# Kernel tuning notes

Hardware: AMD Instinct MI355X
Metric: run time of the kernel (lower is better)

The kernel has to match this reference:

```python
import jax, jax.numpy as jnp
import numpy as np

N = 2_000_000
IN_CH = 10
UNITS = 32  # out_channels // 2 since last_vfe=False
KMAX = 64   # voxel coordinate range per axis


def setup_inputs() -> dict:
    key = jax.random.key(0)
    k1, k2, k3, k4, k5, k6, k7 = jax.random.split(key, 7)
    return {
        "inputs": jax.random.normal(k1, (N, IN_CH), dtype=jnp.float32),
        "mean": jax.random.normal(k2, (N, 6), dtype=jnp.float32),
        "linear_w": jax.random.normal(k3, (IN_CH, UNITS), dtype=jnp.float32) * 0.1,
        "linear_b": jax.random.normal(k4, (UNITS,), dtype=jnp.float32) * 0.1,
        "weight_w": jax.random.normal(k5, (6, UNITS), dtype=jnp.float32) * 0.1,
        "weight_b": jax.random.normal(k6, (UNITS,), dtype=jnp.float32) * 0.1,
        "bxyz_indx": jax.random.randint(k7, (N, 4), 0, KMAX, dtype=jnp.int32),
    }


def _encode_rows(bxyz_indx):
    # unique-by-row is equivalent to unique on a collision-free scalar key;
    # scatter_max-then-gather is invariant to how unique ids are labeled.
    b = bxyz_indx.astype(jnp.int64)
    return ((b[:, 0] * KMAX + b[:, 1]) * KMAX + b[:, 2]) * KMAX + b[:, 3]


def reference(inputs, mean, linear_w, linear_b, weight_w, weight_b, bxyz_indx):
    # x = relu(Linear(inputs)); gating by relu(Linear(mean))  (activate=True, gs=None)
    x = jax.nn.relu(inputs @ linear_w + linear_b)          # [N, UNITS]
    x_weight = jax.nn.relu(mean @ weight_w + weight_b)     # [N, UNITS]
    x = x * x_weight
    # unique voxel id per point -> inverse indices (jit-safe fixed size)
    keys = _encode_rows(bxyz_indx)
    _, inv = jnp.unique(keys, return_inverse=True, size=keys.shape[0], fill_value=-1)
    inv = inv.reshape(-1)
    # scatter_max over voxels, then gather back per point
    max_feature = jax.ops.segment_max(x, inv, num_segments=keys.shape[0])
    gather_max = max_feature[inv, :]                       # [N, UNITS]
    return jnp.concatenate([x, gather_max], axis=1)        # [N, 2*UNITS]
```

## Files before the change

### kernel.cpp

```cpp
#include <hip/hip_runtime.h>
#include <stdint.h>

#define IN_CH   10
#define MEAN_CH 6
#define UNITS   32
#define EMPTY_KEY  ((int)0xAAAAAAAA)
#define MULTI_FLAG 0x40000000

typedef float f32x4 __attribute__((ext_vector_type(4)));

__global__ __launch_bounds__(256) void vfe_hash_insert(
    const int* __restrict__ bxyz, int* __restrict__ keytab,
    unsigned char* __restrict__ multi, int* __restrict__ slots,
    unsigned hmask, int hshift, int nrows)
{
    int row = blockIdx.x * blockDim.x + threadIdx.x;
    if (row >= nrows) return;
    const int4 b = *(const int4*)(bxyz + (size_t)row * 4);
    int key = ((b.x * 64 + b.y) * 64 + b.z) * 64 + b.w;
    unsigned h = ((unsigned)key * 2654435761u) >> hshift;
    h &= hmask;
    while (true) {
        int old = atomicCAS(&keytab[h], EMPTY_KEY, key);
        if (old == EMPTY_KEY) break;
        if (old == key) { multi[h] = 1; break; }
        h = (h + 1) & hmask;
    }
    slots[row] = (int)h;
}

__global__ __launch_bounds__(256) void vfe_compute(
    const float* __restrict__ inputs, const float* __restrict__ mean,
    const float* __restrict__ W1, const float* __restrict__ b1,
    const float* __restrict__ W2, const float* __restrict__ b2,
    int* __restrict__ slots, const unsigned char* __restrict__ multi,
    float* __restrict__ out, int* __restrict__ maxtab, int nrows)
{
    int tid = blockIdx.x * blockDim.x + threadIdx.x;
    int row = tid >> 3;
    int c4  = (tid & 7) * 4;
    if (row >= nrows) return;

    const float* __restrict__ in_row = inputs + (size_t)row * IN_CH;
    const float* __restrict__ mn_row = mean   + (size_t)row * MEAN_CH;

    float4 bb1 = *(const float4*)(b1 + c4);
    float a0 = bb1.x, a1 = bb1.y, a2 = bb1.z, a3 = bb1.w;
#pragma unroll
    for (int k = 0; k < IN_CH; ++k) {
        float v = in_row[k];
        float4 w = *(const float4*)(W1 + k * UNITS + c4);
        a0 = fmaf(v, w.x, a0); a1 = fmaf(v, w.y, a1);
        a2 = fmaf(v, w.z, a2); a3 = fmaf(v, w.w, a3);
    }
    a0 = fmaxf(a0, 0.0f); a1 = fmaxf(a1, 0.0f);
    a2 = fmaxf(a2, 0.0f); a3 = fmaxf(a3, 0.0f);

    float4 bb2 = *(const float4*)(b2 + c4);
    float g0 = bb2.x, g1 = bb2.y, g2 = bb2.z, g3 = bb2.w;
#pragma unroll
    for (int k = 0; k < MEAN_CH; ++k) {
        float v = mn_row[k];
        float4 w = *(const float4*)(W2 + k * UNITS + c4);
        g0 = fmaf(v, w.x, g0); g1 = fmaf(v, w.y, g1);
        g2 = fmaf(v, w.z, g2); g3 = fmaf(v, w.w, g3);
    }
    g0 = fmaxf(g0, 0.0f); g1 = fmaxf(g1, 0.0f);
    g2 = fmaxf(g2, 0.0f); g3 = fmaxf(g3, 0.0f);

    f32x4 x;
    x.x = a0 * g0; x.y = a1 * g1; x.z = a2 * g2; x.w = a3 * g3;

    f32x4* o0 = (f32x4*)(out + (size_t)row * 64 + c4);
    f32x4* o1 = (f32x4*)(out + (size_t)row * 64 + 32 + c4);
    __builtin_nontemporal_store(x, o0);
    __builtin_nontemporal_store(x, o1);

    int slotv = slots[row];
    if (multi[slotv]) {
        int* __restrict__ mt = maxtab + (size_t)slotv * UNITS + c4;
        atomicMax(mt + 0, (int)__float_as_uint(x.x));
        atomicMax(mt + 1, (int)__float_as_uint(x.y));
        atomicMax(mt + 2, (int)__float_as_uint(x.z));
        atomicMax(mt + 3, (int)__float_as_uint(x.w));
        if ((tid & 7) == 0)
            slots[row] = slotv | MULTI_FLAG;
    }
}

__global__ __launch_bounds__(256) void vfe_fixup(
    const int* __restrict__ slots, const int* __restrict__ maxtab,
    float* __restrict__ out, int nrows)
{
    int row = blockIdx.x * blockDim.x + threadIdx.x;
    if (row >= nrows) return;
    int v = slots[row];
    if (!(v & MULTI_FLAG)) return;
    int slot = v & ~MULTI_FLAG;
    const f32x4* src = (const f32x4*)(maxtab + (size_t)slot * UNITS);
    f32x4* dst = (f32x4*)(out + (size_t)row * 64 + 32);
#pragma unroll
    for (int i = 0; i < 8; ++i) dst[i] = src[i];
}

extern "C" void kernel_launch(void* const* d_in, const int* in_sizes, int n_in,
                              void* d_out, int out_size, void* d_ws, size_t ws_size,
                              hipStream_t stream)
{
    const float* inputs = (const float*)d_in[0];
    const float* mean   = (const float*)d_in[1];
    const float* W1     = (const float*)d_in[2];
    const float* b1     = (const float*)d_in[3];
    const float* W2     = (const float*)d_in[4];
    const float* b2     = (const float*)d_in[5];
    const int*   bxyz   = (const int*)d_in[6];
    float* out = (float*)d_out;

    const int nrows = in_sizes[0] / IN_CH;

    unsigned hbits = 22;
    size_t need = ((size_t)1 << hbits) * 4
                + ((size_t)1 << hbits)
                + (size_t)nrows * 4
                + ((size_t)1 << hbits) * UNITS * 4;
    if (need > ws_size) hbits = 21;
    const size_t HSIZE = (size_t)1 << hbits;
    const unsigned hmask = (unsigned)(HSIZE - 1);
    const int hshift = 32 - (int)hbits;

    char* p = (char*)d_ws;
    int* keytab          = (int*)p;           p += HSIZE * 4;
    unsigned char* multi = (unsigned char*)p; p += HSIZE;
    int* slots           = (int*)p;           p += (size_t)nrows * 4;
    int* maxtab          = (int*)p;

    (void)hipMemsetAsync(keytab, 0xAA, HSIZE * 4, stream);
    (void)hipMemsetAsync(multi, 0, HSIZE, stream);

    const int blk = 256;
    vfe_hash_insert<<<(nrows + blk - 1) / blk, blk, 0, stream>>>(
        bxyz, keytab, multi, slots, hmask, hshift, nrows);

    const int total = nrows * 8;
    vfe_compute<<<(total + blk - 1) / blk, blk, 0, stream>>>(
        inputs, mean, W1, b1, W2, b2, slots, multi, out, maxtab, nrows);

    vfe_fixup<<<(nrows + blk - 1) / blk, blk, 0, stream>>>(
        slots, maxtab, out, nrows);
}
```

Measured before the change: 947.2 us.

## Replace full hash insert with direct-indexed byte counters and lazy hashing of duplicates

The first pass now counts occurrences per key in a dense 16M-entry byte-counter array using packed 32-bit atomicAdd, in place of CAS-probing every row into a large hash table. Only rows whose key appears more than once get inserted into a smaller hash table, inside the compute kernel, by one lane per row with the slot broadcast by shuffle. This cuts hash-table size and CAS contention, at the cost of a 16MB memset and a byte counter that overflows past 255 duplicates. Output stores also change from nontemporal to regular stores.

```diff
diff --git a/kernel.cpp b/kernel.cpp
--- a/kernel.cpp
+++ b/kernel.cpp
@@ -4,41 +4,36 @@
 #define IN_CH   10
 #define MEAN_CH 6
 #define UNITS   32
-#define EMPTY_KEY  ((int)0xAAAAAAAA)
-#define MULTI_FLAG 0x40000000
+#define EMPTY_KEY ((int)0xAAAAAAAA)
+#define KEYSPACE  (1 << 24)
 
 typedef float f32x4 __attribute__((ext_vector_type(4)));
 
-__global__ __launch_bounds__(256) void vfe_hash_insert(
-    const int* __restrict__ bxyz, int* __restrict__ keytab,
-    unsigned char* __restrict__ multi, int* __restrict__ slots,
-    unsigned hmask, int hshift, int nrows)
+__global__ __launch_bounds__(256) void vfe_count(
+    const int* __restrict__ bxyz, unsigned* __restrict__ cnt_words,
+    int* __restrict__ keys, int nrows)
 {
     int row = blockIdx.x * blockDim.x + threadIdx.x;
     if (row >= nrows) return;
     const int4 b = *(const int4*)(bxyz + (size_t)row * 4);
     int key = ((b.x * 64 + b.y) * 64 + b.z) * 64 + b.w;
-    unsigned h = ((unsigned)key * 2654435761u) >> hshift;
-    h &= hmask;
-    while (true) {
-        int old = atomicCAS(&keytab[h], EMPTY_KEY, key);
-        if (old == EMPTY_KEY) break;
-        if (old == key) { multi[h] = 1; break; }
-        h = (h + 1) & hmask;
-    }
-    slots[row] = (int)h;
+    keys[row] = key;
+    atomicAdd(&cnt_words[key >> 2], 1u << ((key & 3) * 8));
 }
 
 __global__ __launch_bounds__(256) void vfe_compute(
     const float* __restrict__ inputs, const float* __restrict__ mean,
     const float* __restrict__ W1, const float* __restrict__ b1,
     const float* __restrict__ W2, const float* __restrict__ b2,
-    int* __restrict__ slots, const unsigned char* __restrict__ multi,
-    float* __restrict__ out, int* __restrict__ maxtab, int nrows)
+    const int* __restrict__ keys, const unsigned char* __restrict__ cnt_bytes,
+    int* __restrict__ ktab, int* __restrict__ slotidx,
+    float* __restrict__ out, int* __restrict__ maxtab,
+    unsigned cmask, int cshift, int nrows)
 {
-    int tid = blockIdx.x * blockDim.x + threadIdx.x;
-    int row = tid >> 3;
-    int c4  = (tid & 7) * 4;
+    int tid  = blockIdx.x * blockDim.x + threadIdx.x;
+    int row  = tid >> 3;
+    int lane8 = tid & 7;
+    int c4   = lane8 * 4;
     if (row >= nrows) return;
 
     const float* __restrict__ in_row = inputs + (size_t)row * IN_CH;
@@ -71,33 +66,42 @@
     f32x4 x;
     x.x = a0 * g0; x.y = a1 * g1; x.z = a2 * g2; x.w = a3 * g3;
 
-    f32x4* o0 = (f32x4*)(out + (size_t)row * 64 + c4);
-    f32x4* o1 = (f32x4*)(out + (size_t)row * 64 + 32 + c4);
-    __builtin_nontemporal_store(x, o0);
-    __builtin_nontemporal_store(x, o1);
+    *(f32x4*)(out + (size_t)row * 64 + c4)      = x;
+    *(f32x4*)(out + (size_t)row * 64 + 32 + c4) = x;
 
-    int slotv = slots[row];
-    if (multi[slotv]) {
-        int* __restrict__ mt = maxtab + (size_t)slotv * UNITS + c4;
+    int key = keys[row];
+    if (cnt_bytes[key] > 1) {
+        int slot;
+        if (lane8 == 0) {
+            unsigned h = (((unsigned)key * 2654435761u) >> cshift) & cmask;
+            while (true) {
+                int old = atomicCAS(&ktab[h], EMPTY_KEY, key);
+                if (old == EMPTY_KEY || old == key) break;
+                h = (h + 1) & cmask;
+            }
+            slot = (int)h;
+        }
+        slot = __shfl(slot, 0, 8);
+        int* __restrict__ mt = maxtab + (size_t)slot * UNITS + c4;
         atomicMax(mt + 0, (int)__float_as_uint(x.x));
         atomicMax(mt + 1, (int)__float_as_uint(x.y));
         atomicMax(mt + 2, (int)__float_as_uint(x.z));
         atomicMax(mt + 3, (int)__float_as_uint(x.w));
-        if ((tid & 7) == 0)
-            slots[row] = slotv | MULTI_FLAG;
+        if (lane8 == 0) slotidx[row] = slot;
+    } else {
+        if (lane8 == 0) slotidx[row] = -1;
     }
 }
 
 __global__ __launch_bounds__(256) void vfe_fixup(
-    const int* __restrict__ slots, const int* __restrict__ maxtab,
+    const int* __restrict__ slotidx, const int* __restrict__ maxtab,
     float* __restrict__ out, int nrows)
 {
     int row = blockIdx.x * blockDim.x + threadIdx.x;
     if (row >= nrows) return;
-    int v = slots[row];
-    if (!(v & MULTI_FLAG)) return;
-    int slot = v & ~MULTI_FLAG;
-    const f32x4* src = (const f32x4*)(maxtab + (size_t)slot * UNITS);
+    int s = slotidx[row];
+    if (s < 0) return;
+    const f32x4* src = (const f32x4*)(maxtab + (size_t)s * UNITS);
     f32x4* dst = (f32x4*)(out + (size_t)row * 64 + 32);
 #pragma unroll
     for (int i = 0; i < 8; ++i) dst[i] = src[i];
@@ -118,33 +122,35 @@
 
     const int nrows = in_sizes[0] / IN_CH;
 
-    unsigned hbits = 22;
-    size_t need = ((size_t)1 << hbits) * 4
-                + ((size_t)1 << hbits)
-                + (size_t)nrows * 4
-                + ((size_t)1 << hbits) * UNITS * 4;
-    if (need > ws_size) hbits = 21;
-    const size_t HSIZE = (size_t)1 << hbits;
-    const unsigned hmask = (unsigned)(HSIZE - 1);
-    const int hshift = 32 - (int)hbits;
+    unsigned cbits = 20;
+    size_t need = (size_t)KEYSPACE
+                + ((size_t)1 << cbits) * 4
+                + (size_t)nrows * 4 * 2
+                + ((size_t)1 << cbits) * UNITS * 4;
+    if (need > ws_size) cbits = 19;
+    const size_t CSIZE = (size_t)1 << cbits;
+    const unsigned cmask = (unsigned)(CSIZE - 1);
+    const int cshift = 32 - (int)cbits;
 
     char* p = (char*)d_ws;
-    int* keytab          = (int*)p;           p += HSIZE * 4;
-    unsigned char* multi = (unsigned char*)p; p += HSIZE;
-    int* slots           = (int*)p;           p += (size_t)nrows * 4;
-    int* maxtab          = (int*)p;
+    unsigned* cnt_words = (unsigned*)p;  p += KEYSPACE;
+    int* ktab           = (int*)p;       p += CSIZE * 4;
+    int* keys           = (int*)p;       p += (size_t)nrows * 4;
+    int* slotidx        = (int*)p;       p += (size_t)nrows * 4;
+    int* maxtab         = (int*)p;
 
-    (void)hipMemsetAsync(keytab, 0xAA, HSIZE * 4, stream);
-    (void)hipMemsetAsync(multi, 0, HSIZE, stream);
+    (void)hipMemsetAsync(cnt_words, 0, KEYSPACE, stream);
+    (void)hipMemsetAsync(ktab, 0xAA, CSIZE * 4, stream);
 
     const int blk = 256;
-    vfe_hash_insert<<<(nrows + blk - 1) / blk, blk, 0, stream>>>(
-        bxyz, keytab, multi, slots, hmask, hshift, nrows);
+    vfe_count<<<(nrows + blk - 1) / blk, blk, 0, stream>>>(
+        bxyz, cnt_words, keys, nrows);
 
     const int total = nrows * 8;
     vfe_compute<<<(total + blk - 1) / blk, blk, 0, stream>>>(
-        inputs, mean, W1, b1, W2, b2, slots, multi, out, maxtab, nrows);
+        inputs, mean, W1, b1, W2, b2, keys, (const unsigned char*)cnt_words,
+        ktab, slotidx, out, maxtab, cmask, cshift, nrows);
 
     vfe_fixup<<<(nrows + blk - 1) / blk, blk, 0, stream>>>(
-        slots, maxtab, out, nrows);
+        slotidx, maxtab, out, nrows);
 }
```

After: 931.7 us. Within noise of the previous version (-1.6%).
